# Kernel optimization log

Measured on AMD Instinct MI355X. Metric: run time of the kernel, lower is better.

Reference implementation:

```python
import jax, jax.numpy as jnp
import numpy as np

E, H_HEADS, WS = 512, 16, 8
HEAD_D = E // H_HEADS
LN_EPS = 1e-5


def layernorm(x, g, b):
    mu = jnp.mean(x, axis=-1, keepdims=True)
    var = jnp.mean((x - mu) ** 2, axis=-1, keepdims=True)
    return (x - mu) / jnp.sqrt(var + LN_EPS) * g + b


def setup_inputs() -> dict:
    key = jax.random.key(0)
    ks = jax.random.split(key, 10)
    s = 0.02
    return {
        "x": jax.random.normal(ks[0], (4, 4096, E), jnp.float32),
        "in_proj_w": jax.random.normal(ks[1], (3 * E, E), jnp.float32) * s,
        "in_proj_b": jnp.zeros((3 * E,), jnp.float32),
        "out_w": jax.random.normal(ks[2], (E, E), jnp.float32) * s,
        "out_b": jnp.zeros((E,), jnp.float32),
        "ln1_g": jnp.ones((E,), jnp.float32),
        "ln1_b": jnp.zeros((E,), jnp.float32),
        "w1": jax.random.normal(ks[3], (4 * E, E), jnp.float32) * s,
        "b1": jnp.zeros((4 * E,), jnp.float32),
        "w2": jax.random.normal(ks[4], (E, 4 * E), jnp.float32) * s,
        "b2": jnp.zeros((E,), jnp.float32),
        "ln2_g": jnp.ones((E,), jnp.float32),
        "ln2_b": jnp.zeros((E,), jnp.float32),
        "num_patches_h": 64,
        "num_patches_w": 64,
    }


def reference(x, in_proj_w, in_proj_b, out_w, out_b, ln1_g, ln1_b,
              w1, b1, w2, b2, ln2_g, ln2_b, num_patches_h, num_patches_w):
    B, P, _ = x.shape
    Hp, Wp = num_patches_h, num_patches_w  # 64 divisible by WS -> no padding branch
    nwh, nww = Hp // WS, Wp // WS
    # window partition: (B, Hp, Wp, E) -> (B*nW, WS*WS, E)
    xw = x.reshape(B, nwh, WS, nww, WS, E).transpose(0, 1, 3, 2, 4, 5)
    xw = xw.reshape(B * nwh * nww, WS * WS, E)
    # nn.MultiheadAttention default batch_first=False: axis0 is SEQ (L=B*nW),
    # axis1 is BATCH (N=WS*WS). Reproduce that literal semantics.
    L, N = xw.shape[0], xw.shape[1]
    qkv = xw @ in_proj_w.T + in_proj_b          # (L, N, 3E)
    q, k, v = jnp.split(qkv, 3, axis=-1)
    qh = q.reshape(L, N, H_HEADS, HEAD_D)
    kh = k.reshape(L, N, H_HEADS, HEAD_D)
    vh = v.reshape(L, N, H_HEADS, HEAD_D)
    scale = 1.0 / np.sqrt(HEAD_D)
    scores = jnp.einsum('lnhd,mnhd->nhlm', qh, kh) * scale  # (N, h, L, L)
    attn = jax.nn.softmax(scores, axis=-1)
    o = jnp.einsum('nhlm,mnhd->lnhd', attn, vh).reshape(L, N, E)
    attn_out = o @ out_w.T + out_b
    y = layernorm(xw + attn_out, ln1_g, ln1_b)
    ffn = jax.nn.gelu(y @ w1.T + b1, approximate=False) @ w2.T + b2
    y = layernorm(y + ffn, ln2_g, ln2_b)
    # window unpartition
    y = y.reshape(B, nwh, nww, WS, WS, E).transpose(0, 1, 3, 2, 4, 5)
    return y.reshape(B, Hp * Wp, E)[:, :P, :]
```

## Files before the change

kernel.cpp:

```cpp
#include <hip/hip_runtime.h>
#include <cmath>


typedef _Float16 half8 __attribute__((ext_vector_type(8)));
typedef _Float16 half4v __attribute__((ext_vector_type(4)));
typedef float f32x4 __attribute__((ext_vector_type(4)));

#define GLOBAL_AS(p) ((const __attribute__((address_space(1))) void*)(p))
#define LDS_AS(p) ((__attribute__((address_space(3))) void*)(p))

__device__ __forceinline__ void gload_lds16(const _Float16* g, _Float16* l) {
  __builtin_amdgcn_global_load_lds(GLOBAL_AS(g), LDS_AS(l), 16, 0, 0);
}

__device__ __forceinline__ float wave_sum(float v) {
#pragma unroll
  for (int off = 32; off > 0; off >>= 1) v += __shfl_xor(v, off, 64);
  return v;
}

__device__ __forceinline__ float gelu_fast(float x) {
  const float y = 1.5957691216057308f * (x + 0.044715f * x * x * x);
  const float e = __expf(y);
  const float t = 1.0f - 2.0f / (e + 1.0f);
  return 0.5f * x * (1.0f + t);
}

__global__ __launch_bounds__(256) void castw4_kernel(
    const float* __restrict__ s0, _Float16* __restrict__ d0,
    const float* __restrict__ s1, _Float16* __restrict__ d1,
    const float* __restrict__ s2, _Float16* __restrict__ d2,
    const float* __restrict__ s3, _Float16* __restrict__ d3) {
  int b = blockIdx.x;
  const float* s; _Float16* d;
  if (b < 768) { s = s0; d = d0; }
  else if (b < 1024) { s = s1; d = d1; b -= 768; }
  else if (b < 2048) { s = s2; d = d2; b -= 1024; }
  else { s = s3; d = d3; b -= 2048; }
  const int i = (b * 256 + threadIdx.x) * 4;
  const float4 v = *(const float4*)&s[i];
  half4v o;
  o[0] = (_Float16)v.x; o[1] = (_Float16)v.y; o[2] = (_Float16)v.z; o[3] = (_Float16)v.w;
  *(half4v*)&d[i] = o;
}

__global__ __launch_bounds__(256) void gather_x_kernel(const float* __restrict__ x,
                                                       _Float16* __restrict__ xw) {
  const int idx = blockIdx.x * 256 + threadIdx.x;
  const int t = idx >> 6;
  const int e0 = (idx & 63) << 3;
  const int l = t >> 6, n = t & 63;
  const int bb = l >> 6, wh = (l >> 3) & 7, ww = l & 7;
  const int pi = n >> 3, pj = n & 7;
  const int xrow = (bb * 4096 + (wh * 8 + pi) * 64 + (ww * 8 + pj)) * 512;
  const float4 a = *(const float4*)&x[xrow + e0];
  const float4 b = *(const float4*)&x[xrow + e0 + 4];
  half8 o;
  o[0] = (_Float16)a.x; o[1] = (_Float16)a.y; o[2] = (_Float16)a.z; o[3] = (_Float16)a.w;
  o[4] = (_Float16)b.x; o[5] = (_Float16)b.y; o[6] = (_Float16)b.z; o[7] = (_Float16)b.w;
  *(half8*)&xw[t * 512 + e0] = o;
}

template <int EPI, int WM, int WN, int MREP>
__global__ __launch_bounds__(WM * WN * 64, 2) void gemm_kernel(
    const _Float16* __restrict__ A, const _Float16* __restrict__ B,
    const float* __restrict__ bias, _Float16* __restrict__ C,
    int M, int N, int K) {
  constexpr int BM = WM * MREP * 16;
  constexpr int BN = WN * 64;
  constexpr int NW = WM * WN;
  constexpr int TA = BM * 64, TB = BN * 64;
  constexpr int ALW = BM / (8 * NW);
  constexpr int BLW = BN / (8 * NW);
  __shared__ _Float16 L[2][TA + TB];

  const int tid = threadIdx.x, lane = tid & 63, wave = tid >> 6;
  const int wr = wave / WN, wc = wave % WN;
  const int lr = lane & 15, g = lane >> 4;
  const int bm = blockIdx.x, bn = blockIdx.y;

  const int scol = ((lane & 7) ^ (lane >> 3)) << 3;
  const int srow = lane >> 3;
  const _Float16* Ap = A + (size_t)(bm * BM) * K + scol;
  const _Float16* Bp = B + (size_t)(bn * BN) * K + scol;

  auto stage = [&](int b, int tt) {
    const int koff = tt * 64;
#pragma unroll
    for (int i = 0; i < ALW; ++i) {
      const int r0 = wave * (8 * ALW) + i * 8;
      gload_lds16(Ap + (size_t)(r0 + srow) * K + koff, &L[b][r0 * 64]);
    }
#pragma unroll
    for (int i = 0; i < BLW; ++i) {
      const int r0 = wave * (8 * BLW) + i * 8;
      gload_lds16(Bp + (size_t)(r0 + srow) * K + koff, &L[b][TA + r0 * 64]);
    }
  };

  int aoff[2][MREP], boff[2][4];
#pragma unroll
  for (int kk = 0; kk < 2; ++kk) {
#pragma unroll
    for (int m = 0; m < MREP; ++m) {
      const int row = wr * MREP * 16 + m * 16 + lr;
      aoff[kk][m] = row * 64 + (((kk * 4 + g) ^ (row & 7)) << 3);
    }
#pragma unroll
    for (int n = 0; n < 4; ++n) {
      const int row = wc * 64 + n * 16 + lr;
      boff[kk][n] = TA + row * 64 + (((kk * 4 + g) ^ (row & 7)) << 3);
    }
  }

  f32x4 acc[MREP][4] = {};
  const int NT = K >> 6;

  stage(0, 0);
  stage(1, 1);
  asm volatile("s_waitcnt vmcnt(8)" ::: "memory");
  asm volatile("s_barrier" ::: "memory");

  for (int t = 0; t < NT; ++t) {
    const int p = t & 1;
    const _Float16* Lp = &L[p][0];
#pragma unroll
    for (int kk = 0; kk < 2; ++kk) {
      half8 af[MREP], bf[4];
#pragma unroll
      for (int m = 0; m < MREP; ++m) af[m] = *(const half8*)&Lp[aoff[kk][m]];
#pragma unroll
      for (int n = 0; n < 4; ++n) bf[n] = *(const half8*)&Lp[boff[kk][n]];
      __builtin_amdgcn_s_setprio(1);
#pragma unroll
      for (int m = 0; m < MREP; ++m)
#pragma unroll
        for (int n = 0; n < 4; ++n)
          acc[m][n] = __builtin_amdgcn_mfma_f32_16x16x32_f16(af[m], bf[n], acc[m][n], 0, 0, 0);
      __builtin_amdgcn_s_setprio(0);
    }
    asm volatile("s_waitcnt lgkmcnt(0)" ::: "memory");
    asm volatile("s_barrier" ::: "memory");
    if (t + 2 < NT) stage(p, t + 2);
    if (t + 1 < NT) {
      if (t + 2 < NT) asm volatile("s_waitcnt vmcnt(8)" ::: "memory");
      else            asm volatile("s_waitcnt vmcnt(0)" ::: "memory");
      asm volatile("s_barrier" ::: "memory");
    }
  }

  asm volatile("s_waitcnt lgkmcnt(0)" ::: "memory");
  asm volatile("s_barrier" ::: "memory");

  float bsv[4];
#pragma unroll
  for (int n = 0; n < 4; ++n) bsv[n] = bias[bn * BN + wc * 64 + n * 16 + lr];
  _Float16* Lc = &L[0][0] + wave * (MREP * 16 * 64);
#pragma unroll
  for (int m = 0; m < MREP; ++m)
#pragma unroll
    for (int n = 0; n < 4; ++n)
#pragma unroll
      for (int r = 0; r < 4; ++r) {
        float v = acc[m][n][r] + bsv[n];
        if (EPI == 1) v = gelu_fast(v);
        const int row = m * 16 + g * 4 + r;
        const int col = n * 16 + lr;
        Lc[row * 64 + (col ^ ((row & 7) << 3))] = (_Float16)v;
      }
  const int rrow = lane >> 3, slot = lane & 7;
  const int growb = bm * BM + wr * MREP * 16;
  const int gcol = bn * BN + wc * 64 + slot * 8;
#pragma unroll
  for (int blk = 0; blk < MREP * 2; ++blk) {
    const int row = blk * 8 + rrow;
    const half8 vv = *(const half8*)&Lc[row * 64 + ((slot ^ (row & 7)) << 3)];
    *(half8*)&C[(size_t)(growb + row) * N + gcol] = vv;
  }
}

__global__ __launch_bounds__(256) void attn_kernel(const _Float16* __restrict__ qkv,
                                                   _Float16* __restrict__ o_out) {
  const int n = blockIdx.x & 63;
  const int h = blockIdx.x >> 6;
  __shared__ _Float16 Ksh[256 * 40];
  __shared__ _Float16 Vt[32 * 264];
  __shared__ _Float16 Pw[4 * 64 * 72];
  const int tid = threadIdx.x;
  const int wq = tid >> 6, lane = tid & 63;
  const int lr = lane & 15, g = lane >> 4;
  const int hq = h * 32;

#pragma unroll
  for (int pass = 0; pass < 4; ++pass) {
    const int e = pass * 2048 + tid * 8;
    const int m = e >> 5, d = e & 31;
    const int base = (m * 64 + n) * 1536 + hq;
    const half8 k8 = *(const half8*)&qkv[base + 512 + d];
    const half8 v8 = *(const half8*)&qkv[base + 1024 + d];
    *(half8*)&Ksh[m * 40 + d] = k8;
#pragma unroll
    for (int j = 0; j < 8; ++j) Vt[(d + j) * 264 + m] = v8[j];
  }
  half8 qf[4];
#pragma unroll
  for (int qt = 0; qt < 4; ++qt) {
    const int qg = wq * 64 + qt * 16 + lr;
    qf[qt] = *(const half8*)&qkv[(qg * 64 + n) * 1536 + hq + g * 8];
  }
  __syncthreads();

  f32x4 o[4][2] = {};
  float den[4] = {0.f, 0.f, 0.f, 0.f};
  const float scale = 0.17677669529663687f;
  _Float16* P = &Pw[wq * (64 * 72)];

  for (int it = 0; it < 4; ++it) {
    const int k0 = it * 64;
#pragma unroll
    for (int qt = 0; qt < 4; ++qt) {
#pragma unroll
      for (int kt = 0; kt < 4; ++kt) {
        const half8 kf = *(const half8*)&Ksh[(k0 + kt * 16 + lr) * 40 + g * 8];
        const f32x4 z = {0.f, 0.f, 0.f, 0.f};
        f32x4 st = __builtin_amdgcn_mfma_f32_16x16x32_f16(kf, qf[qt], z, 0, 0, 0);
        const float p0 = __expf(st[0] * scale);
        const float p1 = __expf(st[1] * scale);
        const float p2 = __expf(st[2] * scale);
        const float p3 = __expf(st[3] * scale);
        den[qt] += (p0 + p1) + (p2 + p3);
        half4v w;
        w[0] = (_Float16)p0; w[1] = (_Float16)p1;
        w[2] = (_Float16)p2; w[3] = (_Float16)p3;
        *(half4v*)&P[(qt * 16 + lr) * 72 + kt * 16 + g * 4] = w;
      }
    }
    __syncthreads();
#pragma unroll
    for (int qt = 0; qt < 4; ++qt) {
#pragma unroll
      for (int ks = 0; ks < 2; ++ks) {
        const half8 pf = *(const half8*)&P[(qt * 16 + lr) * 72 + ks * 32 + g * 8];
#pragma unroll
        for (int dt = 0; dt < 2; ++dt) {
          const half8 vf = *(const half8*)&Vt[(dt * 16 + lr) * 264 + k0 + ks * 32 + g * 8];
          o[qt][dt] = __builtin_amdgcn_mfma_f32_16x16x32_f16(pf, vf, o[qt][dt], 0, 0, 0);
        }
      }
    }
    __syncthreads();
  }

#pragma unroll
  for (int qt = 0; qt < 4; ++qt) {
    float dq = den[qt];
    dq += __shfl_xor(dq, 16);
    dq += __shfl_xor(dq, 32);
    const float inv = 1.0f / dq;
#pragma unroll
    for (int r = 0; r < 4; ++r) {
      const float invr = __shfl(inv, g * 4 + r);
      const int qg = wq * 64 + qt * 16 + g * 4 + r;
      const int obase = (qg * 64 + n) * 512 + hq;
#pragma unroll
      for (int dt = 0; dt < 2; ++dt)
        o_out[obase + dt * 16 + lr] = (_Float16)(o[qt][dt][r] * invr);
    }
  }
}

template <int FINAL>
__global__ __launch_bounds__(256) void ln_kernel(
    const float* __restrict__ res32, const _Float16* __restrict__ add16,
    const float* __restrict__ g, const float* __restrict__ b,
    float* __restrict__ out32, _Float16* __restrict__ out16) {
  const int t = blockIdx.x * 4 + (threadIdx.x >> 6);
  const int lane = threadIdx.x & 63;
  const int e0 = lane << 3;
  const int l = t >> 6, n = t & 63;
  const int bb = l >> 6, wh = (l >> 3) & 7, ww = l & 7;
  const int pi = n >> 3, pj = n & 7;
  const int xrow = (bb * 4096 + (wh * 8 + pi) * 64 + (ww * 8 + pj)) * 512;
  const int trow = t * 512;
  const int rbase = (FINAL ? trow : xrow) + e0;
  const float4 ra = *(const float4*)&res32[rbase];
  const float4 rb = *(const float4*)&res32[rbase + 4];
  const half8 a8 = *(const half8*)&add16[trow + e0];
  float v[8];
  v[0] = ra.x + (float)a8[0]; v[1] = ra.y + (float)a8[1];
  v[2] = ra.z + (float)a8[2]; v[3] = ra.w + (float)a8[3];
  v[4] = rb.x + (float)a8[4]; v[5] = rb.y + (float)a8[5];
  v[6] = rb.z + (float)a8[6]; v[7] = rb.w + (float)a8[7];
  float s = 0.f;
#pragma unroll
  for (int e = 0; e < 8; ++e) s += v[e];
  s = wave_sum(s);
  const float mu = s * (1.0f / 512.0f);
  float vs = 0.f;
#pragma unroll
  for (int e = 0; e < 8; ++e) { const float d = v[e] - mu; vs += d * d; }
  vs = wave_sum(vs);
  const float rstd = rsqrtf(vs * (1.0f / 512.0f) + 1e-5f);
  const float4 g1 = *(const float4*)&g[e0];
  const float4 g2 = *(const float4*)&g[e0 + 4];
  const float4 b1 = *(const float4*)&b[e0];
  const float4 b2 = *(const float4*)&b[e0 + 4];
  float y[8];
  y[0] = (v[0] - mu) * rstd * g1.x + b1.x; y[1] = (v[1] - mu) * rstd * g1.y + b1.y;
  y[2] = (v[2] - mu) * rstd * g1.z + b1.z; y[3] = (v[3] - mu) * rstd * g1.w + b1.w;
  y[4] = (v[4] - mu) * rstd * g2.x + b2.x; y[5] = (v[5] - mu) * rstd * g2.y + b2.y;
  y[6] = (v[6] - mu) * rstd * g2.z + b2.z; y[7] = (v[7] - mu) * rstd * g2.w + b2.w;
  if (FINAL) {
    *(float4*)&out32[xrow + e0] = make_float4(y[0], y[1], y[2], y[3]);
    *(float4*)&out32[xrow + e0 + 4] = make_float4(y[4], y[5], y[6], y[7]);
  } else {
    *(float4*)&out32[trow + e0] = make_float4(y[0], y[1], y[2], y[3]);
    *(float4*)&out32[trow + e0 + 4] = make_float4(y[4], y[5], y[6], y[7]);
    half8 o16;
#pragma unroll
    for (int e = 0; e < 8; ++e) o16[e] = (_Float16)y[e];
    *(half8*)&out16[trow + e0] = o16;
  }
}

extern "C" void kernel_launch(void* const* d_in, const int* in_sizes, int n_in,
                              void* d_out, int out_size, void* d_ws, size_t ws_size,
                              hipStream_t stream) {
  const float* x    = (const float*)d_in[0];
  const float* ipw  = (const float*)d_in[1];
  const float* ipb  = (const float*)d_in[2];
  const float* outw = (const float*)d_in[3];
  const float* outb = (const float*)d_in[4];
  const float* ln1g = (const float*)d_in[5];
  const float* ln1b = (const float*)d_in[6];
  const float* w1   = (const float*)d_in[7];
  const float* b1   = (const float*)d_in[8];
  const float* w2   = (const float*)d_in[9];
  const float* b2   = (const float*)d_in[10];
  const float* ln2g = (const float*)d_in[11];
  const float* ln2b = (const float*)d_in[12];
  float* out = (float*)d_out;
  char* ws = (char*)d_ws;

  _Float16* wqkv_h = (_Float16*)(ws + 0);
  _Float16* wout_h = (_Float16*)(ws + 1572864);
  _Float16* w1_h   = (_Float16*)(ws + 2097152);
  _Float16* w2_h   = (_Float16*)(ws + 4194304);
  _Float16* xw_h   = (_Float16*)(ws + 6291456);
  _Float16* qkv_h  = (_Float16*)(ws + 23068672);
  _Float16* attn_h = (_Float16*)(ws + 90177536);
  _Float16* ao_h   = (_Float16*)(ws + 106954752);
  float*    y32    = (float*)(ws + 123731968);
  _Float16* h_h = qkv_h;
  _Float16* f_h = attn_h;
  _Float16* y16 = xw_h;

  castw4_kernel<<<3072, 256, 0, stream>>>(ipw, wqkv_h, outw, wout_h, w1, w1_h, w2, w2_h);
  gather_x_kernel<<<4096, 256, 0, stream>>>(x, xw_h);
  gemm_kernel<0, 2, 4, 8><<<dim3(64, 6), 512, 0, stream>>>(xw_h, wqkv_h, ipb, qkv_h, 16384, 1536, 512);
  attn_kernel<<<1024, 256, 0, stream>>>(qkv_h, attn_h);
  gemm_kernel<0, 2, 2, 4><<<dim3(128, 4), 256, 0, stream>>>(attn_h, wout_h, outb, ao_h, 16384, 512, 512);
  ln_kernel<0><<<4096, 256, 0, stream>>>(x, ao_h, ln1g, ln1b, y32, y16);
  gemm_kernel<1, 2, 4, 8><<<dim3(64, 8), 512, 0, stream>>>(y16, w1_h, b1, h_h, 16384, 2048, 512);
  gemm_kernel<0, 2, 2, 4><<<dim3(128, 4), 256, 0, stream>>>(h_h, w2_h, b2, f_h, 16384, 512, 2048);
  ln_kernel<1><<<4096, 256, 0, stream>>>(y32, f_h, ln2g, ln2b, out, nullptr);
}
```

Before: 229.0 us.

## Rewrite GEMM with triple-buffered LDS, split prefetch, XCD-aware block remap

```diff
diff --git a/kernel.cpp b/kernel.cpp
--- a/kernel.cpp
+++ b/kernel.cpp
@@ -61,103 +61,101 @@
   *(half8*)&xw[t * 512 + e0] = o;
 }
 
-template <int EPI, int WM, int WN, int MREP>
-__global__ __launch_bounds__(WM * WN * 64, 2) void gemm_kernel(
+template <int EPI, int K>
+__global__ __launch_bounds__(512, 2) void gemm8_kernel(
     const _Float16* __restrict__ A, const _Float16* __restrict__ B,
-    const float* __restrict__ bias, _Float16* __restrict__ C,
-    int M, int N, int K) {
-  constexpr int BM = WM * MREP * 16;
-  constexpr int BN = WN * 64;
-  constexpr int NW = WM * WN;
-  constexpr int TA = BM * 64, TB = BN * 64;
-  constexpr int ALW = BM / (8 * NW);
-  constexpr int BLW = BN / (8 * NW);
-  __shared__ _Float16 L[2][TA + TB];
+    const float* __restrict__ bias, _Float16* __restrict__ C, int N) {
+  constexpr int NT = K / 64;
+  constexpr int TA = 256 * 64;
+  constexpr int TB = 128 * 64;
+  constexpr int TT = TA + TB;
+  __shared__ _Float16 L[3][TT];
 
   const int tid = threadIdx.x, lane = tid & 63, wave = tid >> 6;
-  const int wr = wave / WN, wc = wave % WN;
+  const int wr = wave >> 1, wc = wave & 1;
   const int lr = lane & 15, g = lane >> 4;
-  const int bm = blockIdx.x, bn = blockIdx.y;
+
+  const int nbn = N >> 7;
+  const int cpx = gridDim.x >> 3;
+  const int wg = (blockIdx.x & 7) * cpx + (blockIdx.x >> 3);
+  const int bm = wg / nbn, bn = wg % nbn;
 
   const int scol = ((lane & 7) ^ (lane >> 3)) << 3;
   const int srow = lane >> 3;
-  const _Float16* Ap = A + (size_t)(bm * BM) * K + scol;
-  const _Float16* Bp = B + (size_t)(bn * BN) * K + scol;
-
-  auto stage = [&](int b, int tt) {
+  const _Float16* aS = A + (size_t)(bm * 256 + wave * 8 + srow) * K + scol;
+  const _Float16* bS = B + (size_t)(bn * 128 + wave * 8 + srow) * K + scol;
+
+  auto stage = [&](int s, int tt, int h) {
     const int koff = tt * 64;
-#pragma unroll
-    for (int i = 0; i < ALW; ++i) {
-      const int r0 = wave * (8 * ALW) + i * 8;
-      gload_lds16(Ap + (size_t)(r0 + srow) * K + koff, &L[b][r0 * 64]);
-    }
-#pragma unroll
-    for (int i = 0; i < BLW; ++i) {
-      const int r0 = wave * (8 * BLW) + i * 8;
-      gload_lds16(Bp + (size_t)(r0 + srow) * K + koff, &L[b][TA + r0 * 64]);
+    _Float16* Ls = &L[s][0];
+    if (h == 0) {
+      gload_lds16(aS + (size_t)0 * 64 * K + koff, &Ls[(0 * 64 + wave * 8) * 64]);
+      gload_lds16(aS + (size_t)1 * 64 * K + koff, &Ls[(1 * 64 + wave * 8) * 64]);
+      gload_lds16(aS + (size_t)2 * 64 * K + koff, &Ls[(2 * 64 + wave * 8) * 64]);
+    } else {
+      gload_lds16(aS + (size_t)3 * 64 * K + koff, &Ls[(3 * 64 + wave * 8) * 64]);
+      gload_lds16(bS + (size_t)0 * 64 * K + koff, &Ls[TA + (0 * 64 + wave * 8) * 64]);
+      gload_lds16(bS + (size_t)1 * 64 * K + koff, &Ls[TA + (1 * 64 + wave * 8) * 64]);
     }
   };
 
-  int aoff[2][MREP], boff[2][4];
-#pragma unroll
-  for (int kk = 0; kk < 2; ++kk) {
-#pragma unroll
-    for (int m = 0; m < MREP; ++m) {
-      const int row = wr * MREP * 16 + m * 16 + lr;
-      aoff[kk][m] = row * 64 + (((kk * 4 + g) ^ (row & 7)) << 3);
-    }
-#pragma unroll
-    for (int n = 0; n < 4; ++n) {
-      const int row = wc * 64 + n * 16 + lr;
-      boff[kk][n] = TA + row * 64 + (((kk * 4 + g) ^ (row & 7)) << 3);
-    }
-  }
-
-  f32x4 acc[MREP][4] = {};
-  const int NT = K >> 6;
-
-  stage(0, 0);
-  stage(1, 1);
-  asm volatile("s_waitcnt vmcnt(8)" ::: "memory");
+  const int sw0 = ((g ^ (lr & 7)) << 3);
+  const int sw1 = (((4 + g) ^ (lr & 7)) << 3);
+  int arow[4], brow[4];
+#pragma unroll
+  for (int m = 0; m < 4; ++m) arow[m] = (wr * 64 + m * 16 + lr) * 64;
+#pragma unroll
+  for (int n = 0; n < 4; ++n) brow[n] = TA + (wc * 64 + n * 16 + lr) * 64;
+
+  f32x4 acc[4][4] = {};
+
+  stage(0, 0, 0); stage(0, 0, 1);
+  stage(1, 1, 0); stage(1, 1, 1);
+  asm volatile("s_waitcnt vmcnt(6)" ::: "memory");
   asm volatile("s_barrier" ::: "memory");
 
+  int p = 0, s = 2;
   for (int t = 0; t < NT; ++t) {
-    const int p = t & 1;
     const _Float16* Lp = &L[p][0];
-#pragma unroll
-    for (int kk = 0; kk < 2; ++kk) {
-      half8 af[MREP], bf[4];
-#pragma unroll
-      for (int m = 0; m < MREP; ++m) af[m] = *(const half8*)&Lp[aoff[kk][m]];
-#pragma unroll
-      for (int n = 0; n < 4; ++n) bf[n] = *(const half8*)&Lp[boff[kk][n]];
-      __builtin_amdgcn_s_setprio(1);
-#pragma unroll
-      for (int m = 0; m < MREP; ++m)
-#pragma unroll
-        for (int n = 0; n < 4; ++n)
-          acc[m][n] = __builtin_amdgcn_mfma_f32_16x16x32_f16(af[m], bf[n], acc[m][n], 0, 0, 0);
-      __builtin_amdgcn_s_setprio(0);
-    }
+    half8 af[4], bf[4];
+#pragma unroll
+    for (int m = 0; m < 4; ++m) af[m] = *(const half8*)&Lp[arow[m] + sw0];
+#pragma unroll
+    for (int n = 0; n < 4; ++n) bf[n] = *(const half8*)&Lp[brow[n] + sw0];
+    if (t + 2 < NT) stage(s, t + 2, 0);
+    __builtin_amdgcn_s_setprio(1);
+#pragma unroll
+    for (int m = 0; m < 4; ++m)
+#pragma unroll
+      for (int n = 0; n < 4; ++n)
+        acc[m][n] = __builtin_amdgcn_mfma_f32_16x16x32_f16(af[m], bf[n], acc[m][n], 0, 0, 0);
+    __builtin_amdgcn_s_setprio(0);
+#pragma unroll
+    for (int m = 0; m < 4; ++m) af[m] = *(const half8*)&Lp[arow[m] + sw1];
+#pragma unroll
+    for (int n = 0; n < 4; ++n) bf[n] = *(const half8*)&Lp[brow[n] + sw1];
+    if (t + 2 < NT) stage(s, t + 2, 1);
+    __builtin_amdgcn_s_setprio(1);
+#pragma unroll
+    for (int m = 0; m < 4; ++m)
+#pragma unroll
+      for (int n = 0; n < 4; ++n)
+        acc[m][n] = __builtin_amdgcn_mfma_f32_16x16x32_f16(af[m], bf[n], acc[m][n], 0, 0, 0);
+    __builtin_amdgcn_s_setprio(0);
     asm volatile("s_waitcnt lgkmcnt(0)" ::: "memory");
+    if (t + 2 < NT)      asm volatile("s_waitcnt vmcnt(6)" ::: "memory");
+    else if (t + 1 < NT) asm volatile("s_waitcnt vmcnt(0)" ::: "memory");
     asm volatile("s_barrier" ::: "memory");
-    if (t + 2 < NT) stage(p, t + 2);
-    if (t + 1 < NT) {
-      if (t + 2 < NT) asm volatile("s_waitcnt vmcnt(8)" ::: "memory");
-      else            asm volatile("s_waitcnt vmcnt(0)" ::: "memory");
-      asm volatile("s_barrier" ::: "memory");
-    }
-  }
-
-  asm volatile("s_waitcnt lgkmcnt(0)" ::: "memory");
-  asm volatile("s_barrier" ::: "memory");
+    p = (p == 2) ? 0 : p + 1;
+    s = (s == 2) ? 0 : s + 1;
+  }
 
   float bsv[4];
 #pragma unroll
-  for (int n = 0; n < 4; ++n) bsv[n] = bias[bn * BN + wc * 64 + n * 16 + lr];
-  _Float16* Lc = &L[0][0] + wave * (MREP * 16 * 64);
-#pragma unroll
-  for (int m = 0; m < MREP; ++m)
+  for (int n = 0; n < 4; ++n) bsv[n] = bias[bn * 128 + wc * 64 + n * 16 + lr];
+  _Float16* Lc = &L[0][0] + wave * 4096;
+#pragma unroll
+  for (int m = 0; m < 4; ++m)
 #pragma unroll
     for (int n = 0; n < 4; ++n)
 #pragma unroll
@@ -168,14 +166,15 @@
         const int col = n * 16 + lr;
         Lc[row * 64 + (col ^ ((row & 7) << 3))] = (_Float16)v;
       }
+  asm volatile("s_waitcnt lgkmcnt(0)" ::: "memory");
   const int rrow = lane >> 3, slot = lane & 7;
-  const int growb = bm * BM + wr * MREP * 16;
-  const int gcol = bn * BN + wc * 64 + slot * 8;
-#pragma unroll
-  for (int blk = 0; blk < MREP * 2; ++blk) {
+  const int grow = bm * 256 + wr * 64;
+  const int gcol = bn * 128 + wc * 64 + slot * 8;
+#pragma unroll
+  for (int blk = 0; blk < 8; ++blk) {
     const int row = blk * 8 + rrow;
     const half8 vv = *(const half8*)&Lc[row * 64 + ((slot ^ (row & 7)) << 3)];
-    *(half8*)&C[(size_t)(growb + row) * N + gcol] = vv;
+    *(half8*)&C[(size_t)(grow + row) * N + gcol] = vv;
   }
 }
 
@@ -291,11 +290,11 @@
   v[2] = ra.z + (float)a8[2]; v[3] = ra.w + (float)a8[3];
   v[4] = rb.x + (float)a8[4]; v[5] = rb.y + (float)a8[5];
   v[6] = rb.z + (float)a8[6]; v[7] = rb.w + (float)a8[7];
-  float s = 0.f;
-#pragma unroll
-  for (int e = 0; e < 8; ++e) s += v[e];
-  s = wave_sum(s);
-  const float mu = s * (1.0f / 512.0f);
+  float sm = 0.f;
+#pragma unroll
+  for (int e = 0; e < 8; ++e) sm += v[e];
+  sm = wave_sum(sm);
+  const float mu = sm * (1.0f / 512.0f);
   float vs = 0.f;
 #pragma unroll
   for (int e = 0; e < 8; ++e) { const float d = v[e] - mu; vs += d * d; }
@@ -357,11 +356,11 @@
 
   castw4_kernel<<<3072, 256, 0, stream>>>(ipw, wqkv_h, outw, wout_h, w1, w1_h, w2, w2_h);
   gather_x_kernel<<<4096, 256, 0, stream>>>(x, xw_h);
-  gemm_kernel<0, 2, 4, 8><<<dim3(64, 6), 512, 0, stream>>>(xw_h, wqkv_h, ipb, qkv_h, 16384, 1536, 512);
+  gemm8_kernel<0, 512><<<768, 512, 0, stream>>>(xw_h, wqkv_h, ipb, qkv_h, 1536);
   attn_kernel<<<1024, 256, 0, stream>>>(qkv_h, attn_h);
-  gemm_kernel<0, 2, 2, 4><<<dim3(128, 4), 256, 0, stream>>>(attn_h, wout_h, outb, ao_h, 16384, 512, 512);
+  gemm8_kernel<0, 512><<<256, 512, 0, stream>>>(attn_h, wout_h, outb, ao_h, 512);
   ln_kernel<0><<<4096, 256, 0, stream>>>(x, ao_h, ln1g, ln1b, y32, y16);
-  gemm_kernel<1, 2, 4, 8><<<dim3(64, 8), 512, 0, stream>>>(y16, w1_h, b1, h_h, 16384, 2048, 512);
-  gemm_kernel<0, 2, 2, 4><<<dim3(128, 4), 256, 0, stream>>>(h_h, w2_h, b2, f_h, 16384, 512, 2048);
+  gemm8_kernel<1, 512><<<1024, 512, 0, stream>>>(y16, w1_h, b1, h_h, 2048);
+  gemm8_kernel<0, 2048><<<256, 512, 0, stream>>>(h_h, w2_h, b2, f_h, 512);
   ln_kernel<1><<<4096, 256, 0, stream>>>(y32, f_h, ln2g, ln2b, out, nullptr);
 }
```

Measured after the change: 225.6 us. About the same (-1.5%).
